# Performance work log

Measured on AMD Instinct MI355X. Metric: run time of the kernel, lower is better.

Reference implementation:

```python
import jax, jax.numpy as jnp
import numpy as np

AUG_DIMS = 8
ODE_STEPS = 20  # fixed-step RK4 over t in [0, 1]


def _augment(x):
    # concat zeros along last (channel) dim: [B, S, F] -> [B, S, F + AUG_DIMS]
    z = jnp.zeros(x.shape[:-1] + (AUG_DIMS,), dtype=x.dtype)
    return jnp.concatenate([x, z], axis=-1)


def _ode_solve(z0, W, b):
    # dz/dt = z @ W.T + b, integrated with RK4, 20 steps, t: 0 -> 1
    h = 1.0 / ODE_STEPS

    def f(z):
        return z @ W.T + b

    def step(z, _):
        k1 = f(z)
        k2 = f(z + 0.5 * h * k1)
        k3 = f(z + 0.5 * h * k2)
        k4 = f(z + h * k3)
        z = z + (h / 6.0) * (k1 + 2.0 * k2 + 2.0 * k3 + k4)
        return z, None

    z_final, _ = jax.lax.scan(step, z0, None, length=ODE_STEPS)
    return z_final


def setup_inputs() -> dict:
    key = jax.random.key(0)
    ks = jax.random.split(key, 7)
    F_, C_, H_ = 76, 5, 128
    D = F_ + AUG_DIMS  # 84
    x = jax.random.normal(ks[0], (32, 2048, F_), dtype=jnp.float32)
    s = 1.0 / np.sqrt(D)
    W_ode = jax.random.uniform(ks[1], (D, D), minval=-s, maxval=s, dtype=jnp.float32)
    b_ode = jax.random.uniform(ks[2], (D,), minval=-s, maxval=s, dtype=jnp.float32)
    W_pen = jax.random.uniform(ks[3], (H_, D), minval=-s, maxval=s, dtype=jnp.float32)
    b_pen = jax.random.uniform(ks[4], (H_,), minval=-s, maxval=s, dtype=jnp.float32)
    sh = 1.0 / np.sqrt(H_)
    W_fin = jax.random.uniform(ks[5], (C_, H_), minval=-sh, maxval=sh, dtype=jnp.float32)
    b_fin = jax.random.uniform(ks[6], (C_,), minval=-sh, maxval=sh, dtype=jnp.float32)
    return {"x": x, "W_ode": W_ode, "b_ode": b_ode, "W_pen": W_pen,
            "b_pen": b_pen, "W_fin": W_fin, "b_fin": b_fin}


def reference(x, W_ode, b_ode, W_pen, b_pen, W_fin, b_fin):
    z0 = _augment(x)                       # [B, S, 84]
    z = _ode_solve(z0, W_ode, b_ode)       # ODE solve
    z = z + z0                             # skip-add of augmented input
    h = jax.nn.relu(z @ W_pen.T + b_pen)   # [B, S, 128]
    return h @ W_fin.T + b_fin             # [B, S, 5]
```

## Files before the change

### kernel.cpp

```cpp
#include <hip/hip_runtime.h>

#define K_IN 76
#define DD 84
#define HCH 128
#define CCH 5

#define LWF 88

#define OFF_U 0
#define OFF_C (K_IN*HCH)

__device__ __constant__ float CU[9] = {
    1.f, 0.5f, 1.f/6.f, 1.f/24.f, 1.f/120.f, 1.f/720.f, 1.f/5040.f,
    1.f/40320.f, 1.f/362880.f };
__device__ __constant__ float CC[9] = {
    0.5f, 1.f/6.f, 1.f/24.f, 1.f/120.f, 1.f/720.f, 1.f/5040.f,
    1.f/40320.f, 1.f/362880.f, 1.f/3628800.f };

__global__ __launch_bounds__(256) void col_kernel(
    const float* __restrict__ W,
    const float* __restrict__ bode,
    const float* __restrict__ Wpen,
    const float* __restrict__ bpen,
    float* __restrict__ ws)
{
    __shared__ float Wf[DD*LWF];
    __shared__ float S[88];
    __shared__ float cred[88];

    const int tid = threadIdx.x;
    const int j   = blockIdx.x;
    const bool act = (tid < DD);

    for (int e = tid; e < 1764; e += 256) {
        float4 v = ((const float4*)W)[e];
        int r = e / 21, c4 = (e % 21) * 4;
        *(float4*)&Wf[r*LWF + c4] = v;
    }
    if (tid < DD) S[tid] = Wpen[j*DD + tid];
    if (tid >= DD && tid < 88) cred[tid] = 0.f;
    __syncthreads();

    float wcol[DD];
    if (act) {
#pragma unroll
        for (int k = 0; k < DD; ++k) wcol[k] = Wf[k*LWF + tid];
    }
    const float breg = act ? bode[tid] : 0.f;
    const float s0   = act ? S[tid]   : 0.f;
    float uacc = 2.f * s0;
    float cacc = s0;

#pragma unroll 1
    for (int n = 0; n < 9; ++n) {
        float d = 0.f;
        if (act) {
            float a0 = 0.f, a1 = 0.f, a2 = 0.f, a3 = 0.f;
#pragma unroll
            for (int mg = 0; mg < 21; ++mg) {
                const float4 sv = *(const float4*)&S[mg*4];
                a0 = fmaf(sv.x, wcol[mg*4+0], a0);
                a1 = fmaf(sv.y, wcol[mg*4+1], a1);
                a2 = fmaf(sv.z, wcol[mg*4+2], a2);
                a3 = fmaf(sv.w, wcol[mg*4+3], a3);
            }
            d = (a0 + a1) + (a2 + a3);
        }
        __syncthreads();
        if (act) {
            S[tid] = d;
            uacc = fmaf(CU[n], d, uacc);
            cacc = fmaf(CC[n], d, cacc);
        }
        __syncthreads();
    }

    if (tid < K_IN) ws[OFF_U + tid*HCH + j] = uacc;
    if (act) cred[tid] = breg * cacc;
    __syncthreads();
    if (tid == 0) {
        float a0 = 0.f, a1 = 0.f, a2 = 0.f, a3 = 0.f;
#pragma unroll
        for (int mg = 0; mg < 22; ++mg) {
            const float4 v = *(const float4*)&cred[mg*4];
            a0 += v.x; a1 += v.y; a2 += v.z; a3 += v.w;
        }
        ws[OFF_C + j] = bpen[j] + (a0 + a1) + (a2 + a3);
    }
}

__global__ __launch_bounds__(256) void main_kernel(
    const float* __restrict__ x,
    const float* __restrict__ Ug,
    const float* __restrict__ cg,
    const float* __restrict__ Wfin,
    const float* __restrict__ bfin,
    float* __restrict__ out)
{
    __shared__ float Ut[K_IN*HCH];
    __shared__ float xs[128*K_IN];
    __shared__ float Vl[CCH*HCH];

    const int tid = threadIdx.x;
    const int tx = tid & 31, ty = tid >> 5;
    const int T0 = blockIdx.x * 128;

    for (int i = tid; i < (K_IN*HCH)/4; i += 256)
        ((float4*)Ut)[i] = ((const float4*)Ug)[i];
    {
        const float4* xg = (const float4*)(x + (size_t)T0 * K_IN);
        for (int i = tid; i < (128*K_IN)/4; i += 256)
            ((float4*)xs)[i] = xg[i];
    }
    for (int i = tid; i < CCH*HCH; i += 256) Vl[i] = Wfin[i];
    __syncthreads();

    const int j0 = tx*4;
    const int tb = ty*16;
    float acc[16][4];
#pragma unroll
    for (int t = 0; t < 16; ++t)
#pragma unroll
        for (int q = 0; q < 4; ++q) acc[t][q] = 0.f;

    for (int kc = 0; kc < 19; ++kc) {
        const float4 u0 = *(const float4*)&Ut[(4*kc+0)*HCH + j0];
        const float4 u1 = *(const float4*)&Ut[(4*kc+1)*HCH + j0];
        const float4 u2 = *(const float4*)&Ut[(4*kc+2)*HCH + j0];
        const float4 u3 = *(const float4*)&Ut[(4*kc+3)*HCH + j0];
#pragma unroll
        for (int ti = 0; ti < 16; ++ti) {
            const float4 xv = *(const float4*)&xs[(tb+ti)*K_IN + 4*kc];
            acc[ti][0] = fmaf(xv.x, u0.x, acc[ti][0]);
            acc[ti][1] = fmaf(xv.x, u0.y, acc[ti][1]);
            acc[ti][2] = fmaf(xv.x, u0.z, acc[ti][2]);
            acc[ti][3] = fmaf(xv.x, u0.w, acc[ti][3]);
            acc[ti][0] = fmaf(xv.y, u1.x, acc[ti][0]);
            acc[ti][1] = fmaf(xv.y, u1.y, acc[ti][1]);
            acc[ti][2] = fmaf(xv.y, u1.z, acc[ti][2]);
            acc[ti][3] = fmaf(xv.y, u1.w, acc[ti][3]);
            acc[ti][0] = fmaf(xv.z, u2.x, acc[ti][0]);
            acc[ti][1] = fmaf(xv.z, u2.y, acc[ti][1]);
            acc[ti][2] = fmaf(xv.z, u2.z, acc[ti][2]);
            acc[ti][3] = fmaf(xv.z, u2.w, acc[ti][3]);
            acc[ti][0] = fmaf(xv.w, u3.x, acc[ti][0]);
            acc[ti][1] = fmaf(xv.w, u3.y, acc[ti][1]);
            acc[ti][2] = fmaf(xv.w, u3.z, acc[ti][2]);
            acc[ti][3] = fmaf(xv.w, u3.w, acc[ti][3]);
        }
    }

    const float4 cv = *(const float4*)&cg[j0];
    float* opp = xs;
    float* opf = Ut;
    __syncthreads();

    for (int tg = 0; tg < 4; ++tg) {
        float oa[20];
#pragma unroll
        for (int s = 0; s < 4; ++s) {
            const int ti = tg*4 + s;
            const float h0 = fmaxf(acc[ti][0] + cv.x, 0.f);
            const float h1 = fmaxf(acc[ti][1] + cv.y, 0.f);
            const float h2 = fmaxf(acc[ti][2] + cv.z, 0.f);
            const float h3 = fmaxf(acc[ti][3] + cv.w, 0.f);
#pragma unroll
            for (int m = 0; m < CCH; ++m)
                oa[s*5+m] = h0*Vl[m*HCH + j0]     + h1*Vl[m*HCH + j0 + 1]
                          + h2*Vl[m*HCH + j0 + 2] + h3*Vl[m*HCH + j0 + 3];
        }
#pragma unroll
        for (int i = 0; i < 20; ++i) opp[tid*21 + i] = oa[i];
        __syncthreads();
        if (tid < 160) {
            const int typ = tid / 20, rem = tid % 20;
            float s = 0.f;
            for (int xx = 0; xx < 32; ++xx)
                s += opp[(typ*32 + xx)*21 + rem];
            opf[(typ*16 + tg*4)*5 + rem] = s;
        }
        __syncthreads();
    }

    if (tid < 160) {
        const int gi = tid*4;
        float4 v = *(const float4*)&opf[gi];
        v.x += bfin[(gi+0) % 5]; v.y += bfin[(gi+1) % 5];
        v.z += bfin[(gi+2) % 5]; v.w += bfin[(gi+3) % 5];
        *(float4*)&out[(size_t)T0*CCH + gi] = v;
    }
}

extern "C" void kernel_launch(void* const* d_in, const int* in_sizes, int n_in,
                              void* d_out, int out_size, void* d_ws, size_t ws_size,
                              hipStream_t stream)
{
    (void)in_sizes; (void)n_in; (void)out_size; (void)ws_size;
    const float* x    = (const float*)d_in[0];
    const float* Wode = (const float*)d_in[1];
    const float* bode = (const float*)d_in[2];
    const float* Wpen = (const float*)d_in[3];
    const float* bpen = (const float*)d_in[4];
    const float* Wfin = (const float*)d_in[5];
    const float* bfin = (const float*)d_in[6];
    float* out = (float*)d_out;
    float* wsf = (float*)d_ws;

    col_kernel<<<dim3(HCH), dim3(256), 0, stream>>>(Wode, bode, Wpen, bpen, wsf);
    main_kernel<<<dim3(512), dim3(256), 0, stream>>>(x, wsf + OFF_U, wsf + OFF_C,
                                                     Wfin, bfin, out);
}
```

Measured before the change: 36.26 us.

## Shrink column kernel to one wavefront with double-buffered LDS and shuffle reduction

The precompute kernel now runs one 64-lane wavefront per output column. Each lane holds up to two columns of W_ode in registers, loaded directly from global memory instead of staged through shared memory. Double-buffered shared vectors with block-local fences replace the two __syncthreads per power-series iteration, and a wave shuffle reduction replaces the serial single-thread bias sum. The intent is to cut barrier and latency overhead in this small serial kernel. In exchange it doubles register pressure, depends on lockstep execution within a wavefront for correctness, and uses uncoalesced strided global loads for W.

Measured after the change: 34.27 us. -5.5%, faster.

```diff
diff --git a/kernel.cpp b/kernel.cpp
--- a/kernel.cpp
+++ b/kernel.cpp
@@ -4,8 +4,6 @@
 #define DD 84
 #define HCH 128
 #define CCH 5
-
-#define LWF 88
 
 #define OFF_U 0
 #define OFF_C (K_IN*HCH)
@@ -17,76 +15,80 @@
     0.5f, 1.f/6.f, 1.f/24.f, 1.f/120.f, 1.f/720.f, 1.f/5040.f,
     1.f/40320.f, 1.f/362880.f, 1.f/3628800.f };
 
-__global__ __launch_bounds__(256) void col_kernel(
+__global__ __launch_bounds__(64, 1) void col_kernel(
     const float* __restrict__ W,
     const float* __restrict__ bode,
     const float* __restrict__ Wpen,
     const float* __restrict__ bpen,
     float* __restrict__ ws)
 {
-    __shared__ float Wf[DD*LWF];
-    __shared__ float S[88];
-    __shared__ float cred[88];
-
-    const int tid = threadIdx.x;
-    const int j   = blockIdx.x;
-    const bool act = (tid < DD);
-
-    for (int e = tid; e < 1764; e += 256) {
-        float4 v = ((const float4*)W)[e];
-        int r = e / 21, c4 = (e % 21) * 4;
-        *(float4*)&Wf[r*LWF + c4] = v;
-    }
-    if (tid < DD) S[tid] = Wpen[j*DD + tid];
-    if (tid >= DD && tid < 88) cred[tid] = 0.f;
-    __syncthreads();
-
-    float wcol[DD];
-    if (act) {
-#pragma unroll
-        for (int k = 0; k < DD; ++k) wcol[k] = Wf[k*LWF + tid];
-    }
-    const float breg = act ? bode[tid] : 0.f;
-    const float s0   = act ? S[tid]   : 0.f;
-    float uacc = 2.f * s0;
-    float cacc = s0;
-
-#pragma unroll 1
+    __shared__ __align__(16) float Sa[88];
+    __shared__ __align__(16) float Sb[88];
+
+    const int l  = threadIdx.x;
+    const int j  = blockIdx.x;
+    const int i2 = 64 + l;
+    const bool has2 = (l < 20);
+
+    float wc1[DD], wc2[DD];
+#pragma unroll
+    for (int k = 0; k < DD; ++k) wc1[k] = W[k*DD + l];
+    if (has2) {
+#pragma unroll
+        for (int k = 0; k < DD; ++k) wc2[k] = W[k*DD + i2];
+    }
+
+    float s1 = Wpen[j*DD + l];
+    float s2 = has2 ? Wpen[j*DD + i2] : 0.f;
+    const float b1 = bode[l];
+    const float b2 = has2 ? bode[i2] : 0.f;
+
+    Sa[l] = s1;
+    if (has2) Sa[i2] = s2;
+    __threadfence_block();
+
+    float u1 = 2.f*s1, c1 = s1;
+    float u2 = 2.f*s2, c2 = s2;
+
+    const float* Sc = Sa;
+    float*       Sn = Sb;
+#pragma unroll
     for (int n = 0; n < 9; ++n) {
-        float d = 0.f;
-        if (act) {
-            float a0 = 0.f, a1 = 0.f, a2 = 0.f, a3 = 0.f;
-#pragma unroll
-            for (int mg = 0; mg < 21; ++mg) {
-                const float4 sv = *(const float4*)&S[mg*4];
-                a0 = fmaf(sv.x, wcol[mg*4+0], a0);
-                a1 = fmaf(sv.y, wcol[mg*4+1], a1);
-                a2 = fmaf(sv.z, wcol[mg*4+2], a2);
-                a3 = fmaf(sv.w, wcol[mg*4+3], a3);
-            }
-            d = (a0 + a1) + (a2 + a3);
-        }
-        __syncthreads();
-        if (act) {
-            S[tid] = d;
-            uacc = fmaf(CU[n], d, uacc);
-            cacc = fmaf(CC[n], d, cacc);
-        }
-        __syncthreads();
-    }
-
-    if (tid < K_IN) ws[OFF_U + tid*HCH + j] = uacc;
-    if (act) cred[tid] = breg * cacc;
-    __syncthreads();
-    if (tid == 0) {
         float a0 = 0.f, a1 = 0.f, a2 = 0.f, a3 = 0.f;
-#pragma unroll
-        for (int mg = 0; mg < 22; ++mg) {
-            const float4 v = *(const float4*)&cred[mg*4];
-            a0 += v.x; a1 += v.y; a2 += v.z; a3 += v.w;
-        }
-        ws[OFF_C + j] = bpen[j] + (a0 + a1) + (a2 + a3);
-    }
+        float e0 = 0.f, e1 = 0.f, e2 = 0.f, e3 = 0.f;
+#pragma unroll
+        for (int mg = 0; mg < 21; ++mg) {
+            const float4 sv = *(const float4*)&Sc[mg*4];
+            a0 = fmaf(sv.x, wc1[mg*4+0], a0);
+            a1 = fmaf(sv.y, wc1[mg*4+1], a1);
+            a2 = fmaf(sv.z, wc1[mg*4+2], a2);
+            a3 = fmaf(sv.w, wc1[mg*4+3], a3);
+            e0 = fmaf(sv.x, wc2[mg*4+0], e0);
+            e1 = fmaf(sv.y, wc2[mg*4+1], e1);
+            e2 = fmaf(sv.z, wc2[mg*4+2], e2);
+            e3 = fmaf(sv.w, wc2[mg*4+3], e3);
+        }
+        const float d1 = (a0 + a1) + (a2 + a3);
+        const float d2 = (e0 + e1) + (e2 + e3);
+
+        Sn[l] = d1;
+        if (has2) Sn[i2] = d2;
+        __threadfence_block();
+
+        u1 = fmaf(CU[n], d1, u1);  c1 = fmaf(CC[n], d1, c1);
+        u2 = fmaf(CU[n], d2, u2);  c2 = fmaf(CC[n], d2, c2);
+
+        float* t = (float*)Sc; Sc = Sn; Sn = t;
+    }
+
+    if (l < K_IN)            ws[OFF_U + l*HCH + j]  = u1;
+    if (has2 && i2 < K_IN)   ws[OFF_U + i2*HCH + j] = u2;
+
+    float cc = b1*c1 + b2*c2;
+#pragma unroll
+    for (int off = 32; off > 0; off >>= 1)
+        cc += __shfl_down(cc, off, 64);
+    if (l == 0) ws[OFF_C + j] = bpen[j] + cc;
 }
 
 __global__ __launch_bounds__(256) void main_kernel(
@@ -206,7 +208,7 @@
     float* out = (float*)d_out;
     float* wsf = (float*)d_ws;
 
-    col_kernel<<<dim3(HCH), dim3(256), 0, stream>>>(Wode, bode, Wpen, bpen, wsf);
+    col_kernel<<<dim3(HCH), dim3(64), 0, stream>>>(Wode, bode, Wpen, bpen, wsf);
     main_kernel<<<dim3(512), dim3(256), 0, stream>>>(x, wsf + OFF_U, wsf + OFF_C,
                                                      Wfin, bfin, out);
 }
```
